# Performance work log

Measured on AMD Instinct MI355X. Metric: run time of the kernel, lower is better.

Reference implementation:

```python
import jax, jax.numpy as jnp
import numpy as np
import math

B, T, D, DI, DFF, H = 4, 1024, 1024, 256, 4096, 16
S, N, E = 16, 256, 1024          # stat_num, token_num, exemplar_len
STAT_K, TOKEN_K = 8, 16
NEG = -1e6


def setup_inputs() -> dict:
    key = jax.random.key(0)
    ks = jax.random.split(key, 32)
    r = lambda i, shape: jax.random.normal(ks[i], shape, jnp.float32)
    w = lambda i, shape: r(i, shape) * 0.02
    return dict(
        x=r(0, (B, T, D)),
        stat_enc=r(1, (B * S, N, D)),
        exemplar_enc=r(2, (B, E, D)),
        stat_feature=r(3, (B, S, D)),
        intent_embed=r(4, (B, 1, DI)),
        Wq1=w(5, (D, D)), Wk1=w(6, (D, D)), Wv1=w(7, (D, D)), Wo1=w(8, (D, D)),
        Wq_stat=w(9, (D + DI, D)), Wq_token=w(10, (D + DI, D)),
        Wk_stat=w(11, (D, D)), Wk_token=w(12, (D, D)),
        Wv_sel=w(13, (D, D)), Wo_sel=w(14, (D, D)),
        Wq2=w(15, (D + DI, D)), Wk2=w(16, (D, D)), Wv2=w(17, (D, D)), Wo2=w(18, (D, D)),
        Wg=w(19, (2 * D, 1)),
        W1=w(20, (D, DFF)), b1=jnp.zeros((DFF,), jnp.float32),
        W2=w(21, (DFF, D)), b2=jnp.zeros((D,), jnp.float32),
        g1=jnp.ones((D,), jnp.float32), be1=jnp.zeros((D,), jnp.float32),
        g2=jnp.ones((D,), jnp.float32), be2=jnp.zeros((D,), jnp.float32),
        g3=jnp.ones((D,), jnp.float32), be3=jnp.zeros((D,), jnp.float32),
        stat_valid_len=jax.random.randint(ks[22], (B,), 1, S + 1),
        example_valid_len=jax.random.randint(ks[23], (B,), 1, E + 1),
    )


def _ln(x, g, b):
    m = x.mean(-1, keepdims=True)
    v = ((x - m) ** 2).mean(-1, keepdims=True)
    return (x - m) / jnp.sqrt(v + 1e-5) * g + b


def _mha(q, k, v, valid, Wq, Wk, Wv, Wo):
    Bq, Tq, _ = q.shape
    Sk = k.shape[1]
    sp = lambda z: z.reshape(Bq, z.shape[1], H, -1).transpose(0, 2, 1, 3)  # B,H,L,dh
    qh, kh, vh = sp(q @ Wq), sp(k @ Wk), sp(v @ Wv)
    dh = qh.shape[-1]
    sc = jnp.einsum('bhtd,bhsd->bhts', qh, kh) / math.sqrt(dh)
    vl = valid[:, None, None, None] if valid.ndim == 1 else valid[:, None, :, None]
    sc = jnp.where(jnp.arange(Sk)[None, None, None, :] < vl, sc, NEG)
    w = jax.nn.softmax(sc, axis=-1)
    out = jnp.einsum('bhts,bhsd->bhtd', w, vh).transpose(0, 2, 1, 3).reshape(Bq, Tq, -1)
    return out @ Wo


def _scatter_topk(scores, k):
    # keep top-k per row, everything else -> NEG (matches torch topk+scatter)
    shp = scores.shape
    flat = scores.reshape(-1, shp[-1])
    vals, idx = jax.lax.top_k(flat, k)
    out = jnp.full_like(flat, NEG).at[jnp.arange(flat.shape[0])[:, None], idx].set(vals)
    return out.reshape(shp)


def reference(x, stat_enc, exemplar_enc, stat_feature, intent_embed,
              Wq1, Wk1, Wv1, Wo1,
              Wq_stat, Wq_token, Wk_stat, Wk_token, Wv_sel, Wo_sel,
              Wq2, Wk2, Wv2, Wo2, Wg,
              W1, b1, W2, b2,
              g1, be1, g2, be2, g3, be3,
              stat_valid_len, example_valid_len):
    # masked self-attention (training mode -> causal valid lens)
    dec_valid = jnp.broadcast_to(jnp.arange(1, T + 1)[None, :], (B, T))
    x2 = _mha(x, x, x, dec_valid, Wq1, Wk1, Wv1, Wo1)
    y = _ln(x + x2, g1, be1)
    yi = jnp.concatenate([y, jnp.broadcast_to(intent_embed, (B, T, DI))], axis=-1)

    # selective hierarchical top-k attention
    qs = yi @ Wq_stat                      # [B,T,D]
    qt = yi @ Wq_token                     # [B,T,D]
    ks = stat_feature @ Wk_stat            # [B,S,D]
    kt = (stat_enc @ Wk_token).reshape(B, S, N, D)
    vv = (stat_enc @ Wv_sel).reshape(B, S, N, D)
    scale = math.sqrt(D)
    ssc = jnp.einsum('btd,bsd->bts', qs, ks) / scale
    ssc = jnp.where(jnp.arange(S)[None, None, :] < stat_valid_len[:, None, None], ssc, NEG)
    sw = jax.nn.softmax(_scatter_topk(ssc, min(S - 1, STAT_K)), axis=-1)   # [B,T,S]
    tsc = jnp.einsum('btd,bsnd->btsn', qt, kt) / scale                      # [B,T,S,N]
    tw = jax.nn.softmax(_scatter_topk(tsc, min(N - 1, TOKEN_K)), axis=-1)
    comb = sw[..., None] * tw                                               # [B,T,S,N]
    y2s = jnp.einsum('btsn,bsnd->btd', comb, vv) @ Wo_sel

    # exemplar cross-attention
    y2e = _mha(yi, exemplar_enc, exemplar_enc, example_valid_len, Wq2, Wk2, Wv2, Wo2)

    gate = jax.nn.sigmoid(jnp.concatenate([y2s, y2e], axis=-1) @ Wg)
    y2 = gate * y2s + (1.0 - gate) * y2e
    z = _ln(y + 2.0 * y2, g2, be2)
    ffn = jax.nn.relu(z @ W1 + b1) @ W2 + b2
    return _ln(z + ffn, g3, be3)
```

## Files before the change

### kernel.cpp

```cpp
#include <hip/hip_runtime.h>

typedef unsigned short u16;
typedef short s16x8 __attribute__((ext_vector_type(8)));
typedef u16 u16x4 __attribute__((ext_vector_type(4)));
typedef float f32x4 __attribute__((ext_vector_type(4)));

#define T_N   1024
#define NEGV  -1e6f
#define MB    (1L << 20)

__device__ __forceinline__ u16 f2bf(float f) {
    unsigned u = __float_as_uint(f);
    u += 0x7fffu + ((u >> 16) & 1u);
    return (u16)(u >> 16);
}
__device__ __forceinline__ float bf2f(u16 h) {
    return __uint_as_float(((unsigned)h) << 16);
}
__device__ __forceinline__ f32x4 mfma16(s16x8 a, s16x8 b, f32x4 c) {
    return __builtin_amdgcn_mfma_f32_16x16x32_bf16(a, b, c, 0, 0, 0);
}
__device__ __forceinline__ void gll16(const u16* g, u16* l) {
    __builtin_amdgcn_global_load_lds((const __attribute__((address_space(1))) void*)g,
                                     (__attribute__((address_space(3))) void*)l, 16, 0, 0);
}

struct P6 { const float* s[6]; u16* d[6]; };

__global__ __launch_bounds__(256) void transpose_cast_batch(P6 pp, int K, int N) {
    const float* __restrict__ src = pp.s[blockIdx.z];
    u16* __restrict__ dst = pp.d[blockIdx.z];
    __shared__ float tile[32][33];
    int nb = blockIdx.x * 32, kb = blockIdx.y * 32;
    int tx = threadIdx.x & 31, ty = threadIdx.x >> 5;
    #pragma unroll
    for (int i = 0; i < 4; i++)
        tile[ty + 8*i][tx] = src[(long)(kb + ty + 8*i) * N + nb + tx];
    __syncthreads();
    #pragma unroll
    for (int i = 0; i < 4; i++)
        dst[(long)(nb + ty + 8*i) * K + kb + tx] = f2bf(tile[tx][ty + 8*i]);
}

__global__ __launch_bounds__(256) void cast_bf16_kernel(const float* __restrict__ src,
                                                        u16* __restrict__ dst, long n) {
    long i = ((long)blockIdx.x * 256 + threadIdx.x) * 4;
    if (i >= n) return;
    float4 v = *(const float4*)(src + i);
    u16x4 o = { f2bf(v.x), f2bf(v.y), f2bf(v.z), f2bf(v.w) };
    *(u16x4*)(dst + i) = o;
}

template<typename OutT, bool RELU, bool HAS_BIAS>
__global__ __launch_bounds__(256) void gemm_bt(
    const u16* __restrict__ A, const u16* __restrict__ Bt, OutT* __restrict__ C,
    const float* __restrict__ bias, int M, int N, int K,
    int lda, int ldb, int ldc,
    int batchDivA, long sA, long sB, long sC)
{
    A  += (long)(blockIdx.z / batchDivA) * sA;
    Bt += (long)blockIdx.z * sB;
    C  += (long)blockIdx.z * sC;
    __shared__ __align__(16) u16 As[4096];
    __shared__ __align__(16) u16 Bs[4096];
    const int tid = threadIdx.x;
    const int wave = tid >> 6, lane = tid & 63;
    const int quad = lane >> 4, l16 = lane & 15;
    const int wr = (wave >> 1) * 64, wc = (wave & 1) * 64;
    const long row0 = (long)blockIdx.y * 128, col0 = (long)blockIdx.x * 128;

    f32x4 acc[4][4] = {};

    const int l4r = lane >> 2;
    const int l4c = (lane & 3) * 8;
    const int ra = wave * 32 + l4r;
    const u16* Ap0 = A + (row0 + ra) * (long)lda + l4c;
    const u16* Ap1 = Ap0 + 16L * lda;
    const u16* Bp0 = Bt + (col0 + ra) * (long)ldb + l4c;
    const u16* Bp1 = Bp0 + 16L * ldb;
    u16* AsW0 = &As[(wave * 32) * 32];
    u16* AsW1 = &As[(wave * 32 + 16) * 32];
    u16* BsW0 = &Bs[(wave * 32) * 32];
    u16* BsW1 = &Bs[(wave * 32 + 16) * 32];
    const bool aok0 = (row0 + wave * 32) < M;
    const bool aok1 = (row0 + wave * 32 + 16) < M;

    for (int k0 = 0; k0 < K; k0 += 32) {
        __syncthreads();
        if (aok0) gll16(Ap0 + k0, AsW0);
        if (aok1) gll16(Ap1 + k0, AsW1);
        gll16(Bp0 + k0, BsW0);
        gll16(Bp1 + k0, BsW1);
        __syncthreads();
        s16x8 af[4], bfr[4];
        #pragma unroll
        for (int i = 0; i < 4; i++)
            af[i]  = *(const s16x8*)&As[(wr + i*16 + l16) * 32 + quad*8];
        #pragma unroll
        for (int j = 0; j < 4; j++)
            bfr[j] = *(const s16x8*)&Bs[(wc + j*16 + l16) * 32 + quad*8];
        #pragma unroll
        for (int i = 0; i < 4; i++)
            #pragma unroll
            for (int j = 0; j < 4; j++)
                acc[i][j] = mfma16(af[i], bfr[j], acc[i][j]);
    }

    #pragma unroll
    for (int i = 0; i < 4; i++) {
        long row = row0 + wr + i*16 + quad*4;
        #pragma unroll
        for (int j = 0; j < 4; j++) {
            long col = col0 + wc + j*16 + l16;
            float bv = 0.f;
            if constexpr (HAS_BIAS) bv = bias[col];
            #pragma unroll
            for (int r = 0; r < 4; r++) {
                if (row + r < M) {
                    float v = acc[i][j][r] + bv;
                    if constexpr (RELU) v = fmaxf(v, 0.f);
                    if constexpr (sizeof(OutT) == 2) C[(row + r) * (long)ldc + col] = f2bf(v);
                    else                             C[(row + r) * (long)ldc + col] = v;
                }
            }
        }
    }
}

template<bool CAUSAL>
__global__ __launch_bounds__(256) void flash_attn_kernel(
    const u16* __restrict__ Q, const u16* __restrict__ Kg, const u16* __restrict__ Vg,
    const int* __restrict__ valid_len, u16* __restrict__ O,
    int qld, int kld, int vld)
{
    const int h = blockIdx.y, b = blockIdx.z;
    const int qt0 = blockIdx.x * 64;
    const int tid = threadIdx.x;
    const int wave = tid >> 6, lane = tid & 63;
    const int quad = lane >> 4, l16 = lane & 15;

    __shared__ __align__(16) u16 Qs[64][72];
    __shared__ __align__(16) u16 Ks[64][72];
    __shared__ __align__(16) u16 Vt[64][72];
    __shared__ __align__(16) u16 Ps[4][16][72];

    const int sr = tid >> 2, scc = (tid & 3) * 16;
    {
        const u16* qp = Q + ((long)b * T_N + qt0 + sr) * qld + h * 64 + scc;
        *(s16x8*)&Qs[sr][scc]     = *(const s16x8*)qp;
        *(s16x8*)&Qs[sr][scc + 8] = *(const s16x8*)(qp + 8);
    }
    float m_i[4] = {-1e30f, -1e30f, -1e30f, -1e30f};
    float l_i[4] = {0.f, 0.f, 0.f, 0.f};
    f32x4 o_acc[4] = {};

    int vl = 0, kend;
    if (CAUSAL) kend = qt0 + 64;
    else { vl = valid_len[b]; kend = (vl + 63) & ~63; }

    for (int kv0 = 0; kv0 < kend; kv0 += 64) {
        __syncthreads();
        {
            const u16* kp = Kg + ((long)b * T_N + kv0 + sr) * kld + h * 64 + scc;
            *(s16x8*)&Ks[sr][scc]     = *(const s16x8*)kp;
            *(s16x8*)&Ks[sr][scc + 8] = *(const s16x8*)(kp + 8);
            const u16* vp = Vg + ((long)b * T_N + kv0 + sr) * vld + h * 64 + scc;
            s16x8 v0 = *(const s16x8*)vp;
            s16x8 v1 = *(const s16x8*)(vp + 8);
            #pragma unroll
            for (int j = 0; j < 8; j++) {
                Vt[scc + j][sr]     = (u16)v0[j];
                Vt[scc + 8 + j][sr] = (u16)v1[j];
            }
        }
        __syncthreads();
        f32x4 sc[4] = {};
        #pragma unroll
        for (int kk = 0; kk < 64; kk += 32) {
            s16x8 aq = *(const s16x8*)&Qs[wave*16 + l16][kk + quad*8];
            #pragma unroll
            for (int j = 0; j < 4; j++) {
                s16x8 bk = *(const s16x8*)&Ks[j*16 + l16][kk + quad*8];
                sc[j] = mfma16(aq, bk, sc[j]);
            }
        }
        const int qrow = qt0 + wave*16 + quad*4;
        #pragma unroll
        for (int j = 0; j < 4; j++) {
            int kcol = kv0 + j*16 + l16;
            #pragma unroll
            for (int r = 0; r < 4; r++) {
                float s = sc[j][r] * 0.125f;
                bool ok = CAUSAL ? (kcol <= qrow + r) : (kcol < vl);
                sc[j][r] = ok ? s : -1e30f;
            }
        }
        float alpha[4];
        #pragma unroll
        for (int r = 0; r < 4; r++) {
            float mx = fmaxf(fmaxf(sc[0][r], sc[1][r]), fmaxf(sc[2][r], sc[3][r]));
            #pragma unroll
            for (int d = 1; d < 16; d <<= 1) mx = fmaxf(mx, __shfl_xor(mx, d, 64));
            float mn = fmaxf(m_i[r], mx);
            alpha[r] = __expf(m_i[r] - mn);
            m_i[r] = mn;
        }
        float rsum[4] = {0.f, 0.f, 0.f, 0.f};
        #pragma unroll
        for (int j = 0; j < 4; j++)
            #pragma unroll
            for (int r = 0; r < 4; r++) {
                float pv = __expf(sc[j][r] - m_i[r]);
                sc[j][r] = pv;
                rsum[r] += pv;
            }
        #pragma unroll
        for (int r = 0; r < 4; r++) {
            #pragma unroll
            for (int d = 1; d < 16; d <<= 1) rsum[r] += __shfl_xor(rsum[r], d, 64);
            l_i[r] = l_i[r] * alpha[r] + rsum[r];
        }
        #pragma unroll
        for (int j = 0; j < 4; j++)
            #pragma unroll
            for (int r = 0; r < 4; r++)
                Ps[wave][quad*4 + r][j*16 + l16] = f2bf(sc[j][r]);
        #pragma unroll
        for (int j2 = 0; j2 < 4; j2++)
            #pragma unroll
            for (int r = 0; r < 4; r++)
                o_acc[j2][r] *= alpha[r];
        __syncthreads();
        #pragma unroll
        for (int kk = 0; kk < 64; kk += 32) {
            s16x8 ap = *(const s16x8*)&Ps[wave][l16][kk + quad*8];
            #pragma unroll
            for (int j2 = 0; j2 < 4; j2++) {
                s16x8 bv = *(const s16x8*)&Vt[j2*16 + l16][kk + quad*8];
                o_acc[j2] = mfma16(ap, bv, o_acc[j2]);
            }
        }
    }
    #pragma unroll
    for (int j2 = 0; j2 < 4; j2++) {
        #pragma unroll
        for (int r = 0; r < 4; r++) {
            float v = o_acc[j2][r] / l_i[r];
            long row = (long)b * T_N + qt0 + wave*16 + quad*4 + r;
            O[row * 1024 + h*64 + j2*16 + l16] = f2bf(v);
        }
    }
}

__global__ __launch_bounds__(256) void ssc_kernel(
    const u16* __restrict__ qs, const u16* __restrict__ ks,
    const int* __restrict__ svl, float* __restrict__ ssc, int qld)
{
    const int t = blockIdx.x, b = blockIdx.y;
    const int wave = threadIdx.x >> 6, lane = threadIdx.x & 63;
    const u16* qrow = qs + ((long)b * T_N + t) * qld + lane * 16;
    const int vl = svl[b];
    for (int s = wave; s < 16; s += 4) {
        const u16* krow = ks + ((long)b * 16 + s) * 1024 + lane * 16;
        float acc = 0.f;
        #pragma unroll
        for (int seg = 0; seg < 2; seg++) {
            s16x8 qv = *(const s16x8*)(qrow + seg*8);
            s16x8 kv = *(const s16x8*)(krow + seg*8);
            #pragma unroll
            for (int j = 0; j < 8; j++) acc += bf2f((u16)qv[j]) * bf2f((u16)kv[j]);
        }
        #pragma unroll
        for (int d = 1; d < 64; d <<= 1) acc += __shfl_xor(acc, d, 64);
        if (lane == 0)
            ssc[((long)b * T_N + t) * 16 + s] = (s < vl) ? acc * (1.f/32.f) : NEGV;
    }
}

__global__ __launch_bounds__(256) void select_combine_kernel(
    const float* __restrict__ ssc, const float* __restrict__ tsc,
    const u16* __restrict__ vv, u16* __restrict__ out, int t0, int vld)
{
    const int tl = blockIdx.x, b = blockIdx.y;
    const int tg = t0 + tl;
    const int tid = threadIdx.x;
    const int wave = tid >> 6, lane = tid & 63;
    __shared__ float coeff[128];
    __shared__ long  rowoff[128];
    __shared__ int   sel_s[8];
    __shared__ float sel_w[8];

    if (wave == 0) {
        float cur = (lane < 16) ? ssc[((long)b * T_N + tg) * 16 + lane] : -3e38f;
        float mx0 = 0.f, ssum = 0.f, myv = -3e38f;
        int myi = 0;
        #pragma unroll
        for (int it = 0; it < 8; it++) {
            float mv = cur; int mi = lane;
            #pragma unroll
            for (int d = 1; d < 64; d <<= 1) {
                float ov = __shfl_xor(mv, d, 64);
                int   oi = __shfl_xor(mi, d, 64);
                if (ov > mv || (ov == mv && oi < mi)) { mv = ov; mi = oi; }
            }
            if (it == 0) mx0 = mv;
            ssum += __expf(mv - mx0);
            if (lane == it) { myv = mv; myi = mi; }
            if (lane == mi) cur = -3e38f;
        }
        if (lane < 8) { sel_s[lane] = myi; sel_w[lane] = __expf(myv - mx0) / ssum; }
    }
    __syncthreads();

    for (int slot = wave; slot < 8; slot += 4) {
        int s = sel_s[slot];
        float sw = sel_w[slot];
        const float* trow = tsc + (((long)b * 16 + s) * 512 + tl) * 256;
        float4 lv4 = *(const float4*)(trow + lane * 4);
        float loc[4] = { lv4.x, lv4.y, lv4.z, lv4.w };
        float mx0 = 0.f, tsum = 0.f, myv = -3e38f;
        int myi = 0;
        for (int it = 0; it < 16; it++) {
            float mv = -3e38f; int mi = 0;
            #pragma unroll
            for (int u = 0; u < 4; u++)
                if (loc[u] > mv) { mv = loc[u]; mi = lane*4 + u; }
            #pragma unroll
            for (int d = 1; d < 64; d <<= 1) {
                float ov = __shfl_xor(mv, d, 64);
                int   oi = __shfl_xor(mi, d, 64);
                if (ov > mv || (ov == mv && oi < mi)) { mv = ov; mi = oi; }
            }
            if (it == 0) mx0 = mv * (1.f/32.f);
            tsum += __expf(mv * (1.f/32.f) - mx0);
            if (lane == it) { myv = mv; myi = mi; }
            if ((mi >> 2) == lane) {
                int u = mi & 3;
                if (u == 0) loc[0] = -3e38f;
                else if (u == 1) loc[1] = -3e38f;
                else if (u == 2) loc[2] = -3e38f;
                else loc[3] = -3e38f;
            }
        }
        if (lane < 16) {
            coeff[slot * 16 + lane]  = sw * __expf(myv * (1.f/32.f) - mx0) / tsum;
            rowoff[slot * 16 + lane] = (long)((b * 16 + s) * 256 + myi) * vld;
        }
    }
    __syncthreads();

    const int d0 = tid * 4;
    float a0 = 0.f, a1 = 0.f, a2 = 0.f, a3 = 0.f;
    for (int r = 0; r < 128; r++) {
        float c = coeff[r];
        const u16* vp = vv + rowoff[r] + d0;
        u16x4 v4 = *(const u16x4*)vp;
        a0 += c * bf2f(v4[0]);
        a1 += c * bf2f(v4[1]);
        a2 += c * bf2f(v4[2]);
        a3 += c * bf2f(v4[3]);
    }
    u16x4 o4 = { f2bf(a0), f2bf(a1), f2bf(a2), f2bf(a3) };
    *(u16x4*)(out + ((long)b * T_N + tg) * 1024 + d0) = o4;
}

__device__ __forceinline__ float block_sum(float v, float* red) {
    #pragma unroll
    for (int d = 1; d < 64; d <<= 1) v += __shfl_xor(v, d, 64);
    __syncthreads();
    if ((threadIdx.x & 63) == 0) red[threadIdx.x >> 6] = v;
    __syncthreads();
    return red[0] + red[1] + red[2] + red[3];
}

__global__ __launch_bounds__(256) void ln1_kernel(
    const float* __restrict__ x, const float* __restrict__ x2,
    const float* __restrict__ intent, const float* __restrict__ g, const float* __restrict__ be,
    u16* __restrict__ yi)
{
    __shared__ float red[4];
    const long row = blockIdx.x;
    const int tid = threadIdx.x;
    const long base = row * 1024 + tid * 4;
    float4 xv = *(const float4*)(x + base);
    float4 dv = *(const float4*)(x2 + base);
    float h0 = xv.x + dv.x, h1 = xv.y + dv.y, h2 = xv.z + dv.z, h3 = xv.w + dv.w;
    float s1 = block_sum(h0 + h1 + h2 + h3, red);
    float s2 = block_sum(h0*h0 + h1*h1 + h2*h2 + h3*h3, red);
    float mean = s1 * (1.f/1024.f);
    float var = s2 * (1.f/1024.f) - mean * mean;
    float inv = rsqrtf(var + 1e-5f);
    const int c = tid * 4;
    float4 gv = *(const float4*)(g + c);
    float4 bv = *(const float4*)(be + c);
    float o0 = (h0 - mean) * inv * gv.x + bv.x;
    float o1 = (h1 - mean) * inv * gv.y + bv.y;
    float o2 = (h2 - mean) * inv * gv.z + bv.z;
    float o3 = (h3 - mean) * inv * gv.w + bv.w;
    u16x4 ob = { f2bf(o0), f2bf(o1), f2bf(o2), f2bf(o3) };
    *(u16x4*)(yi + row * 1280 + c) = ob;
    const int b = (int)(row >> 10);
    yi[row * 1280 + 1024 + tid] = f2bf(intent[b * 256 + tid]);
}

__global__ __launch_bounds__(256) void gate_ln2_kernel(
    const u16* __restrict__ yi, const float* __restrict__ y2s, const float* __restrict__ y2e,
    const float* __restrict__ Wg, const float* __restrict__ g, const float* __restrict__ be,
    float* __restrict__ z, u16* __restrict__ zbf)
{
    __shared__ float red[4];
    const long row = blockIdx.x;
    const int tid = threadIdx.x;
    const long base = row * 1024 + tid * 4;
    const int c = tid * 4;
    float4 sv = *(const float4*)(y2s + base);
    float4 ev = *(const float4*)(y2e + base);
    float4 w1 = *(const float4*)(Wg + c);
    float4 w2 = *(const float4*)(Wg + 1024 + c);
    float dot = sv.x*w1.x + sv.y*w1.y + sv.z*w1.z + sv.w*w1.w
              + ev.x*w2.x + ev.y*w2.y + ev.z*w2.z + ev.w*w2.w;
    float tot = block_sum(dot, red);
    float gate = 1.f / (1.f + __expf(-tot));
    u16x4 yv4 = *(const u16x4*)(yi + row * 1280 + c);
    float h0 = bf2f(yv4[0]) + 2.f * (gate * sv.x + (1.f - gate) * ev.x);
    float h1 = bf2f(yv4[1]) + 2.f * (gate * sv.y + (1.f - gate) * ev.y);
    float h2 = bf2f(yv4[2]) + 2.f * (gate * sv.z + (1.f - gate) * ev.z);
    float h3 = bf2f(yv4[3]) + 2.f * (gate * sv.w + (1.f - gate) * ev.w);
    float s1 = block_sum(h0 + h1 + h2 + h3, red);
    float s2 = block_sum(h0*h0 + h1*h1 + h2*h2 + h3*h3, red);
    float mean = s1 * (1.f/1024.f);
    float var = s2 * (1.f/1024.f) - mean * mean;
    float inv = rsqrtf(var + 1e-5f);
    float4 gv = *(const float4*)(g + c);
    float4 bv = *(const float4*)(be + c);
    float o0 = (h0 - mean) * inv * gv.x + bv.x;
    float o1 = (h1 - mean) * inv * gv.y + bv.y;
    float o2 = (h2 - mean) * inv * gv.z + bv.z;
    float o3 = (h3 - mean) * inv * gv.w + bv.w;
    *(float4*)(z + base) = make_float4(o0, o1, o2, o3);
    u16x4 ob = { f2bf(o0), f2bf(o1), f2bf(o2), f2bf(o3) };
    *(u16x4*)(zbf + row * 1024 + c) = ob;
}

__global__ __launch_bounds__(256) void ln3_kernel(
    const float* __restrict__ z, const float* __restrict__ p0, const float* __restrict__ p1,
    const float* __restrict__ b2,
    const float* __restrict__ g, const float* __restrict__ be, float* __restrict__ out)
{
    __shared__ float red[4];
    const long row = blockIdx.x;
    const int tid = threadIdx.x;
    const long base = row * 1024 + tid * 4;
    const int c = tid * 4;
    float4 zv = *(const float4*)(z + base);
    float4 f0 = *(const float4*)(p0 + base);
    float4 f1 = *(const float4*)(p1 + base);
    float4 bb = *(const float4*)(b2 + c);
    float h0 = zv.x + f0.x + f1.x + bb.x;
    float h1 = zv.y + f0.y + f1.y + bb.y;
    float h2 = zv.z + f0.z + f1.z + bb.z;
    float h3 = zv.w + f0.w + f1.w + bb.w;
    float s1 = block_sum(h0 + h1 + h2 + h3, red);
    float s2 = block_sum(h0*h0 + h1*h1 + h2*h2 + h3*h3, red);
    float mean = s1 * (1.f/1024.f);
    float var = s2 * (1.f/1024.f) - mean * mean;
    float inv = rsqrtf(var + 1e-5f);
    float4 gv = *(const float4*)(g + c);
    float4 bv = *(const float4*)(be + c);
    float o0 = (h0 - mean) * inv * gv.x + bv.x;
    float o1 = (h1 - mean) * inv * gv.y + bv.y;
    float o2 = (h2 - mean) * inv * gv.z + bv.z;
    float o3 = (h3 - mean) * inv * gv.w + bv.w;
    *(float4*)(out + base) = make_float4(o0, o1, o2, o3);
}

extern "C" void kernel_launch(void* const* d_in, const int* in_sizes, int n_in,
                              void* d_out, int out_size, void* d_ws, size_t ws_size,
                              hipStream_t stream)
{
    (void)in_sizes; (void)n_in; (void)out_size; (void)ws_size;
    const float* x      = (const float*)d_in[0];
    const float* stat_e = (const float*)d_in[1];
    const float* exem   = (const float*)d_in[2];
    const float* sfeat  = (const float*)d_in[3];
    const float* intent = (const float*)d_in[4];
    const float* Wg  = (const float*)d_in[19];
    const float* b1  = (const float*)d_in[21];
    const float* b2  = (const float*)d_in[23];
    const float* g1  = (const float*)d_in[24]; const float* be1 = (const float*)d_in[25];
    const float* g2  = (const float*)d_in[26]; const float* be2 = (const float*)d_in[27];
    const float* g3  = (const float*)d_in[28]; const float* be3 = (const float*)d_in[29];
    const int* svl = (const int*)d_in[30];
    const int* evl = (const int*)d_in[31];
    float* outp = (float*)d_out;

    char* base = (char*)d_ws;
    u16*  bufA  = (u16*)(base + 0*MB);
    u16*  qkv1  = (u16*)(base + 8*MB);
    float* x2a  = (float*)(base + 8*MB);
    u16*  kv2   = (u16*)(base + 8*MB);
    u16*  w1t   = (u16*)(base + 8*MB);
    u16*  w2t   = (u16*)(base + 16*MB);
    u16*  yibf  = (u16*)(base + 32*MB);
    u16*  buf3  = (u16*)(base + 42*MB);
    u16*  zbf   = (u16*)(base + 42*MB);
    u16*  sebf  = (u16*)(base + 66*MB);
    float* tsch = (float*)(base + 66*MB);
    u16*  hid   = (u16*)(base + 66*MB);
    u16*  ktvv  = (u16*)(base + 98*MB);
    float* y2sf = (float*)(base + 98*MB);
    float* p0f  = (float*)(base + 98*MB);
    u16*  exbf  = (u16*)(base + 114*MB);
    float* y2ef = (float*)(base + 122*MB);
    float* zf   = (float*)(base + 138*MB);
    u16*  sfbf  = (u16*)(base + 162*MB);
    u16*  ksbf  = (u16*)(base + 162*MB + 256*1024);
    float* sscf = (float*)(base + 162*MB + 512*1024);
    char* wpool = base + 163*MB;

    dim3 blk(256);
    auto cast = [&](const float* s, u16* d, long n) {
        cast_bf16_kernel<<<dim3((unsigned)((n/4 + 255) / 256)), blk, 0, stream>>>(s, d, n);
    };
    auto g_n = [&](const u16* A, const u16* Bt, u16* C, int M, int N, int K,
                   int lda, int ldb, int ldc) {
        gemm_bt<u16,false,false><<<dim3(N/128, (M+127)/128, 1), blk, 0, stream>>>(
            A, Bt, C, nullptr, M, N, K, lda, ldb, ldc, 1, 0, 0, 0);
    };
    auto g_f = [&](const u16* A, const u16* Bt, float* C, int M, int N, int K,
                   int lda, int ldb, int ldc) {
        gemm_bt<float,false,false><<<dim3(N/128, (M+127)/128, 1), blk, 0, stream>>>(
            A, Bt, C, nullptr, M, N, K, lda, ldb, ldc, 1, 0, 0, 0);
    };

    u16* wqkv1t = (u16*)wpool;
    u16* wo1t   = (u16*)(wpool) + 3L*1024*1024;
    {
        P6 pp{};
        pp.s[0]=(const float*)d_in[5]; pp.d[0]=wqkv1t;
        pp.s[1]=(const float*)d_in[6]; pp.d[1]=wqkv1t + 1L*1024*1024;
        pp.s[2]=(const float*)d_in[7]; pp.d[2]=wqkv1t + 2L*1024*1024;
        pp.s[3]=(const float*)d_in[8]; pp.d[3]=wo1t;
        transpose_cast_batch<<<dim3(32, 32, 4), blk, 0, stream>>>(pp, 1024, 1024);
    }
    cast(x, bufA, 4096L*1024);
    g_n(bufA, wqkv1t, qkv1, 4096, 3072, 1024, 1024, 1024, 3072);
    flash_attn_kernel<true><<<dim3(16, 16, 4), blk, 0, stream>>>(
        qkv1, qkv1 + 1024, qkv1 + 2048, nullptr, bufA, 3072, 3072, 3072);
    g_f(bufA, wo1t, x2a, 4096, 1024, 1024, 1024, 1024, 1024);
    ln1_kernel<<<dim3(4096), blk, 0, stream>>>(x, x2a, intent, g1, be1, yibf);

    u16* wq3t = (u16*)wpool;
    {
        P6 pp{};
        pp.s[0]=(const float*)d_in[9];  pp.d[0]=wq3t;
        pp.s[1]=(const float*)d_in[10]; pp.d[1]=wq3t + 1L*1024*1280;
        pp.s[2]=(const float*)d_in[15]; pp.d[2]=wq3t + 2L*1024*1280;
        transpose_cast_batch<<<dim3(32, 40, 3), blk, 0, stream>>>(pp, 1280, 1024);
    }
    g_n(yibf, wq3t, buf3, 4096, 3072, 1280, 1280, 1280, 3072);
    u16* wkst = (u16*)wpool;
    u16* wkv  = (u16*)(wpool) + 1L*1024*1024;
    {
        P6 pp{};
        pp.s[0]=(const float*)d_in[11]; pp.d[0]=wkst;
        pp.s[1]=(const float*)d_in[12]; pp.d[1]=wkv;
        pp.s[2]=(const float*)d_in[13]; pp.d[2]=wkv + 1L*1024*1024;
        transpose_cast_batch<<<dim3(32, 32, 3), blk, 0, stream>>>(pp, 1024, 1024);
    }
    cast(sfeat, sfbf, 64L*1024);
    cast(stat_e, sebf, 16384L*1024);
    g_n(sfbf, wkst, ksbf, 64, 1024, 1024, 1024, 1024, 1024);
    g_n(sebf, wkv, ktvv, 16384, 2048, 1024, 1024, 1024, 2048);
    ssc_kernel<<<dim3(1024, 4), blk, 0, stream>>>(buf3, ksbf, svl, sscf, 3072);
    for (int hh = 0; hh < 2; hh++) {
        long t0 = hh * 512;
        gemm_bt<float,false,false><<<dim3(2, 4, 64), blk, 0, stream>>>(
            buf3 + 1024 + t0*3072, ktvv, tsch, nullptr, 512, 256, 1024,
            3072, 2048, 256, 16, (long)T_N*3072, 256L*2048, 512L*256);
        select_combine_kernel<<<dim3(512, 4), blk, 0, stream>>>(
            sscf, tsch, ktvv + 1024, bufA, (int)t0, 2048);
    }
    u16* wost = (u16*)wpool;
    u16* wkv2 = (u16*)(wpool) + 1L*1024*1024;
    u16* wo2t = (u16*)(wpool) + 3L*1024*1024;
    {
        P6 pp{};
        pp.s[0]=(const float*)d_in[14]; pp.d[0]=wost;
        pp.s[1]=(const float*)d_in[16]; pp.d[1]=wkv2;
        pp.s[2]=(const float*)d_in[17]; pp.d[2]=wkv2 + 1L*1024*1024;
        pp.s[3]=(const float*)d_in[18]; pp.d[3]=wo2t;
        transpose_cast_batch<<<dim3(32, 32, 4), blk, 0, stream>>>(pp, 1024, 1024);
    }
    g_f(bufA, wost, y2sf, 4096, 1024, 1024, 1024, 1024, 1024);

    cast(exem, exbf, 4096L*1024);
    g_n(exbf, wkv2, kv2, 4096, 2048, 1024, 1024, 1024, 2048);
    flash_attn_kernel<false><<<dim3(16, 16, 4), blk, 0, stream>>>(
        buf3 + 2048, kv2, kv2 + 1024, evl, bufA, 3072, 2048, 2048);
    g_f(bufA, wo2t, y2ef, 4096, 1024, 1024, 1024, 1024, 1024);

    gate_ln2_kernel<<<dim3(4096), blk, 0, stream>>>(yibf, y2sf, y2ef, Wg, g2, be2, zf, zbf);

    {
        P6 pp{}; pp.s[0] = (const float*)d_in[20]; pp.d[0] = w1t;
        transpose_cast_batch<<<dim3(128, 32, 1), blk, 0, stream>>>(pp, 1024, 4096);
    }
    {
        P6 pp{}; pp.s[0] = (const float*)d_in[22]; pp.d[0] = w2t;
        transpose_cast_batch<<<dim3(32, 128, 1), blk, 0, stream>>>(pp, 4096, 1024);
    }
    gemm_bt<u16,true,true><<<dim3(32, 32, 1), blk, 0, stream>>>(
        zbf, w1t, hid, b1, 4096, 4096, 1024, 1024, 1024, 4096, 1, 0, 0, 0);
    gemm_bt<float,false,false><<<dim3(8, 32, 2), blk, 0, stream>>>(
        hid, w2t, p0f, nullptr, 4096, 1024, 2048, 4096, 4096, 1024,
        1, 2048, 2048, 4096L*1024);

    ln3_kernel<<<dim3(4096), blk, 0, stream>>>(zf, p0f, p0f + 4096L*1024, b2, g3, be3, outp);
}
```

Baseline: 1.032 ms.

## Split-K output projections, batch weight casts, and swizzle GEMM block order

The three 1024x1024 output-projection GEMMs (attention, selection, exemplar) each become two half-K launches writing partial fp32 sums, and the following LayerNorm/gate kernels add the partials. This raises the block count from 256 to 512 per projection for better CU occupancy. Weight transpose-casts and input casts are merged into fewer batched launches with per-slice shapes, and the GEMM gets a grid swizzle of the block index to improve L2 reuse. The workspace layout is reshuffled to hold the extra partial buffers, which costs extra memory traffic for the partial outputs.

```diff
diff --git a/kernel.cpp b/kernel.cpp
--- a/kernel.cpp
+++ b/kernel.cpp
@@ -25,13 +25,16 @@
                                      (__attribute__((address_space(3))) void*)l, 16, 0, 0);
 }
 
-struct P6 { const float* s[6]; u16* d[6]; };
-
-__global__ __launch_bounds__(256) void transpose_cast_batch(P6 pp, int K, int N) {
-    const float* __restrict__ src = pp.s[blockIdx.z];
-    u16* __restrict__ dst = pp.d[blockIdx.z];
+struct T8 { const float* s[8]; u16* d[8]; int K[8]; int N[8]; };
+
+__global__ __launch_bounds__(256) void transpose_cast_b(T8 pp) {
+    const int z = blockIdx.z;
+    const int K = pp.K[z], N = pp.N[z];
+    int nb = blockIdx.x * 32, kb = blockIdx.y * 32;
+    if (nb >= N || kb >= K) return;
+    const float* __restrict__ src = pp.s[z];
+    u16* __restrict__ dst = pp.d[z];
     __shared__ float tile[32][33];
-    int nb = blockIdx.x * 32, kb = blockIdx.y * 32;
     int tx = threadIdx.x & 31, ty = threadIdx.x >> 5;
     #pragma unroll
     for (int i = 0; i < 4; i++)
@@ -42,6 +45,18 @@
         dst[(long)(nb + ty + 8*i) * K + kb + tx] = f2bf(tile[tx][ty + 8*i]);
 }
 
+struct C4 { const float* s[4]; u16* d[4]; long n[4]; };
+
+__global__ __launch_bounds__(256) void cast_batch_kernel(C4 c) {
+    long i = ((long)blockIdx.x * 256 + threadIdx.x) * 4;
+    if (i >= c.n[blockIdx.z]) return;
+    const float* __restrict__ src = c.s[blockIdx.z];
+    u16* __restrict__ dst = c.d[blockIdx.z];
+    float4 v = *(const float4*)(src + i);
+    u16x4 o = { f2bf(v.x), f2bf(v.y), f2bf(v.z), f2bf(v.w) };
+    *(u16x4*)(dst + i) = o;
+}
+
 __global__ __launch_bounds__(256) void cast_bf16_kernel(const float* __restrict__ src,
                                                         u16* __restrict__ dst, long n) {
     long i = ((long)blockIdx.x * 256 + threadIdx.x) * 4;
@@ -61,13 +76,25 @@
     A  += (long)(blockIdx.z / batchDivA) * sA;
     Bt += (long)blockIdx.z * sB;
     C  += (long)blockIdx.z * sC;
+
+    int bx = blockIdx.x, by = blockIdx.y;
+    {
+        const int nb = gridDim.x * gridDim.y;
+        if ((nb & 7) == 0) {
+            int flat = by * gridDim.x + bx;
+            int nf = (flat & 7) * (nb >> 3) + (flat >> 3);
+            bx = nf % gridDim.x;
+            by = nf / gridDim.x;
+        }
+    }
+
     __shared__ __align__(16) u16 As[4096];
     __shared__ __align__(16) u16 Bs[4096];
     const int tid = threadIdx.x;
     const int wave = tid >> 6, lane = tid & 63;
     const int quad = lane >> 4, l16 = lane & 15;
     const int wr = (wave >> 1) * 64, wc = (wave & 1) * 64;
-    const long row0 = (long)blockIdx.y * 128, col0 = (long)blockIdx.x * 128;
+    const long row0 = (long)by * 128, col0 = (long)bx * 128;
 
     f32x4 acc[4][4] = {};
 
@@ -374,7 +401,7 @@
 }
 
 __global__ __launch_bounds__(256) void ln1_kernel(
-    const float* __restrict__ x, const float* __restrict__ x2,
+    const float* __restrict__ x, const float* __restrict__ p0, const float* __restrict__ p1,
     const float* __restrict__ intent, const float* __restrict__ g, const float* __restrict__ be,
     u16* __restrict__ yi)
 {
@@ -383,8 +410,10 @@
     const int tid = threadIdx.x;
     const long base = row * 1024 + tid * 4;
     float4 xv = *(const float4*)(x + base);
-    float4 dv = *(const float4*)(x2 + base);
-    float h0 = xv.x + dv.x, h1 = xv.y + dv.y, h2 = xv.z + dv.z, h3 = xv.w + dv.w;
+    float4 d0 = *(const float4*)(p0 + base);
+    float4 d1 = *(const float4*)(p1 + base);
+    float h0 = xv.x + d0.x + d1.x, h1 = xv.y + d0.y + d1.y;
+    float h2 = xv.z + d0.z + d1.z, h3 = xv.w + d0.w + d1.w;
     float s1 = block_sum(h0 + h1 + h2 + h3, red);
     float s2 = block_sum(h0*h0 + h1*h1 + h2*h2 + h3*h3, red);
     float mean = s1 * (1.f/1024.f);
@@ -404,7 +433,9 @@
 }
 
 __global__ __launch_bounds__(256) void gate_ln2_kernel(
-    const u16* __restrict__ yi, const float* __restrict__ y2s, const float* __restrict__ y2e,
+    const u16* __restrict__ yi,
+    const float* __restrict__ s0p, const float* __restrict__ s1p,
+    const float* __restrict__ e0p, const float* __restrict__ e1p,
     const float* __restrict__ Wg, const float* __restrict__ g, const float* __restrict__ be,
     float* __restrict__ z, u16* __restrict__ zbf)
 {
@@ -413,8 +444,12 @@
     const int tid = threadIdx.x;
     const long base = row * 1024 + tid * 4;
     const int c = tid * 4;
-    float4 sv = *(const float4*)(y2s + base);
-    float4 ev = *(const float4*)(y2e + base);
+    float4 sa = *(const float4*)(s0p + base);
+    float4 sb = *(const float4*)(s1p + base);
+    float4 ea = *(const float4*)(e0p + base);
+    float4 eb = *(const float4*)(e1p + base);
+    float4 sv = make_float4(sa.x + sb.x, sa.y + sb.y, sa.z + sb.z, sa.w + sb.w);
+    float4 ev = make_float4(ea.x + eb.x, ea.y + eb.y, ea.z + eb.z, ea.w + eb.w);
     float4 w1 = *(const float4*)(Wg + c);
     float4 w2 = *(const float4*)(Wg + 1024 + c);
     float dot = sv.x*w1.x + sv.y*w1.y + sv.z*w1.z + sv.w*w1.w
@@ -497,79 +532,87 @@
     char* base = (char*)d_ws;
     u16*  bufA  = (u16*)(base + 0*MB);
     u16*  qkv1  = (u16*)(base + 8*MB);
-    float* x2a  = (float*)(base + 8*MB);
+    float* p0x  = (float*)(base + 8*MB);
+    u16*  wq3t  = (u16*)(base + 8*MB);
+    u16*  wkst  = (u16*)(base + 8*MB + 7864320L);
+    u16*  wkv   = (u16*)(base + 8*MB + 9961472L);
+    u16*  wost  = (u16*)(base + 8*MB + 14155776L);
     u16*  kv2   = (u16*)(base + 8*MB);
-    u16*  w1t   = (u16*)(base + 8*MB);
-    u16*  w2t   = (u16*)(base + 16*MB);
+    float* zf   = (float*)(base + 8*MB);
     u16*  yibf  = (u16*)(base + 32*MB);
+    float* p1x  = (float*)(base + 42*MB);
     u16*  buf3  = (u16*)(base + 42*MB);
     u16*  zbf   = (u16*)(base + 42*MB);
+    u16*  w1t   = (u16*)(base + 50*MB);
+    u16*  w2t   = (u16*)(base + 58*MB);
     u16*  sebf  = (u16*)(base + 66*MB);
     float* tsch = (float*)(base + 66*MB);
     u16*  hid   = (u16*)(base + 66*MB);
     u16*  ktvv  = (u16*)(base + 98*MB);
-    float* y2sf = (float*)(base + 98*MB);
-    float* p0f  = (float*)(base + 98*MB);
-    u16*  exbf  = (u16*)(base + 114*MB);
-    float* y2ef = (float*)(base + 122*MB);
-    float* zf   = (float*)(base + 138*MB);
+    float* ys0  = (float*)(base + 98*MB);
+    float* ys1  = (float*)(base + 114*MB);
+    float* ye0  = (float*)(base + 130*MB);
+    float* ye1  = (float*)(base + 146*MB);
+    float* f0p  = (float*)(base + 98*MB);
     u16*  sfbf  = (u16*)(base + 162*MB);
     u16*  ksbf  = (u16*)(base + 162*MB + 256*1024);
     float* sscf = (float*)(base + 162*MB + 512*1024);
     char* wpool = base + 163*MB;
 
     dim3 blk(256);
-    auto cast = [&](const float* s, u16* d, long n) {
-        cast_bf16_kernel<<<dim3((unsigned)((n/4 + 255) / 256)), blk, 0, stream>>>(s, d, n);
-    };
     auto g_n = [&](const u16* A, const u16* Bt, u16* C, int M, int N, int K,
                    int lda, int ldb, int ldc) {
         gemm_bt<u16,false,false><<<dim3(N/128, (M+127)/128, 1), blk, 0, stream>>>(
             A, Bt, C, nullptr, M, N, K, lda, ldb, ldc, 1, 0, 0, 0);
     };
-    auto g_f = [&](const u16* A, const u16* Bt, float* C, int M, int N, int K,
-                   int lda, int ldb, int ldc) {
-        gemm_bt<float,false,false><<<dim3(N/128, (M+127)/128, 1), blk, 0, stream>>>(
-            A, Bt, C, nullptr, M, N, K, lda, ldb, ldc, 1, 0, 0, 0);
+    auto g_sk = [&](const u16* A, const u16* Bt, float* P, int lda) {
+        gemm_bt<float,false,false><<<dim3(8, 32, 2), blk, 0, stream>>>(
+            A, Bt, P, nullptr, 4096, 1024, 512, lda, 1024, 1024,
+            1, 512, 512, 4096L*1024);
     };
+
+    {
+        C4 cc{};
+        cc.s[0] = stat_e; cc.d[0] = sebf; cc.n[0] = 16384L*1024;
+        cc.s[1] = x;      cc.d[1] = bufA; cc.n[1] = 4096L*1024;
+        cc.s[2] = sfeat;  cc.d[2] = sfbf; cc.n[2] = 64L*1024;
+        cast_batch_kernel<<<dim3(16384, 1, 3), blk, 0, stream>>>(cc);
+    }
 
     u16* wqkv1t = (u16*)wpool;
     u16* wo1t   = (u16*)(wpool) + 3L*1024*1024;
     {
-        P6 pp{};
+        T8 pp{};
         pp.s[0]=(const float*)d_in[5]; pp.d[0]=wqkv1t;
         pp.s[1]=(const float*)d_in[6]; pp.d[1]=wqkv1t + 1L*1024*1024;
         pp.s[2]=(const float*)d_in[7]; pp.d[2]=wqkv1t + 2L*1024*1024;
         pp.s[3]=(const float*)d_in[8]; pp.d[3]=wo1t;
-        transpose_cast_batch<<<dim3(32, 32, 4), blk, 0, stream>>>(pp, 1024, 1024);
-    }
-    cast(x, bufA, 4096L*1024);
+        for (int i = 0; i < 4; i++) { pp.K[i] = 1024; pp.N[i] = 1024; }
+        transpose_cast_b<<<dim3(32, 32, 4), blk, 0, stream>>>(pp);
+    }
     g_n(bufA, wqkv1t, qkv1, 4096, 3072, 1024, 1024, 1024, 3072);
     flash_attn_kernel<true><<<dim3(16, 16, 4), blk, 0, stream>>>(
         qkv1, qkv1 + 1024, qkv1 + 2048, nullptr, bufA, 3072, 3072, 3072);
-    g_f(bufA, wo1t, x2a, 4096, 1024, 1024, 1024, 1024, 1024);
-    ln1_kernel<<<dim3(4096), blk, 0, stream>>>(x, x2a, intent, g1, be1, yibf);
-
-    u16* wq3t = (u16*)wpool;
-    {
-        P6 pp{};
-        pp.s[0]=(const float*)d_in[9];  pp.d[0]=wq3t;
-        pp.s[1]=(const float*)d_in[10]; pp.d[1]=wq3t + 1L*1024*1280;
-        pp.s[2]=(const float*)d_in[15]; pp.d[2]=wq3t + 2L*1024*1280;
-        transpose_cast_batch<<<dim3(32, 40, 3), blk, 0, stream>>>(pp, 1280, 1024);
+    {
+        gemm_bt<float,false,false><<<dim3(8, 32, 1), blk, 0, stream>>>(
+            bufA, wo1t, p0x, nullptr, 4096, 1024, 512, 1024, 1024, 1024, 1, 0, 0, 0);
+        gemm_bt<float,false,false><<<dim3(8, 32, 1), blk, 0, stream>>>(
+            bufA + 512, wo1t + 512, p1x, nullptr, 4096, 1024, 512, 1024, 1024, 1024, 1, 0, 0, 0);
+    }
+    ln1_kernel<<<dim3(4096), blk, 0, stream>>>(x, p0x, p1x, intent, g1, be1, yibf);
+
+    {
+        T8 pp{};
+        pp.s[0]=(const float*)d_in[9];  pp.d[0]=wq3t;                    pp.K[0]=1280; pp.N[0]=1024;
+        pp.s[1]=(const float*)d_in[10]; pp.d[1]=wq3t + 1L*1024*1280;     pp.K[1]=1280; pp.N[1]=1024;
+        pp.s[2]=(const float*)d_in[15]; pp.d[2]=wq3t + 2L*1024*1280;     pp.K[2]=1280; pp.N[2]=1024;
+        pp.s[3]=(const float*)d_in[11]; pp.d[3]=wkst;                    pp.K[3]=1024; pp.N[3]=1024;
+        pp.s[4]=(const float*)d_in[12]; pp.d[4]=wkv;                     pp.K[4]=1024; pp.N[4]=1024;
+        pp.s[5]=(const float*)d_in[13]; pp.d[5]=wkv + 1L*1024*1024;      pp.K[5]=1024; pp.N[5]=1024;
+        pp.s[6]=(const float*)d_in[14]; pp.d[6]=wost;                    pp.K[6]=1024; pp.N[6]=1024;
+        transpose_cast_b<<<dim3(32, 40, 7), blk, 0, stream>>>(pp);
     }
     g_n(yibf, wq3t, buf3, 4096, 3072, 1280, 1280, 1280, 3072);
-    u16* wkst = (u16*)wpool;
-    u16* wkv  = (u16*)(wpool) + 1L*1024*1024;
-    {
-        P6 pp{};
-        pp.s[0]=(const float*)d_in[11]; pp.d[0]=wkst;
-        pp.s[1]=(const float*)d_in[12]; pp.d[1]=wkv;
-        pp.s[2]=(const float*)d_in[13]; pp.d[2]=wkv + 1L*1024*1024;
-        transpose_cast_batch<<<dim3(32, 32, 3), blk, 0, stream>>>(pp, 1024, 1024);
-    }
-    cast(sfeat, sfbf, 64L*1024);
-    cast(stat_e, sebf, 16384L*1024);
     g_n(sfbf, wkst, ksbf, 64, 1024, 1024, 1024, 1024, 1024);
     g_n(sebf, wkv, ktvv, 16384, 2048, 1024, 1024, 1024, 2048);
     ssc_kernel<<<dim3(1024, 4), blk, 0, stream>>>(buf3, ksbf, svl, sscf, 3072);
@@ -581,40 +624,52 @@
         select_combine_kernel<<<dim3(512, 4), blk, 0, stream>>>(
             sscf, tsch, ktvv + 1024, bufA, (int)t0, 2048);
     }
-    u16* wost = (u16*)wpool;
-    u16* wkv2 = (u16*)(wpool) + 1L*1024*1024;
-    u16* wo2t = (u16*)(wpool) + 3L*1024*1024;
-    {
-        P6 pp{};
-        pp.s[0]=(const float*)d_in[14]; pp.d[0]=wost;
-        pp.s[1]=(const float*)d_in[16]; pp.d[1]=wkv2;
-        pp.s[2]=(const float*)d_in[17]; pp.d[2]=wkv2 + 1L*1024*1024;
-        pp.s[3]=(const float*)d_in[18]; pp.d[3]=wo2t;
-        transpose_cast_batch<<<dim3(32, 32, 4), blk, 0, stream>>>(pp, 1024, 1024);
-    }
-    g_f(bufA, wost, y2sf, 4096, 1024, 1024, 1024, 1024, 1024);
-
-    cast(exem, exbf, 4096L*1024);
-    g_n(exbf, wkv2, kv2, 4096, 2048, 1024, 1024, 1024, 2048);
+    {
+        gemm_bt<float,false,false><<<dim3(8, 32, 1), blk, 0, stream>>>(
+            bufA, wost, ys0, nullptr, 4096, 1024, 512, 1024, 1024, 1024, 1, 0, 0, 0);
+        gemm_bt<float,false,false><<<dim3(8, 32, 1), blk, 0, stream>>>(
+            bufA + 512, wost + 512, ys1, nullptr, 4096, 1024, 512, 1024, 1024, 1024, 1, 0, 0, 0);
+    }
+
+    u16* wkv2 = (u16*)wpool;
+    u16* wo2t = (u16*)(wpool) + 2L*1024*1024;
+    {
+        T8 pp{};
+        pp.s[0]=(const float*)d_in[16]; pp.d[0]=wkv2;
+        pp.s[1]=(const float*)d_in[17]; pp.d[1]=wkv2 + 1L*1024*1024;
+        pp.s[2]=(const float*)d_in[18]; pp.d[2]=wo2t;
+        for (int i = 0; i < 3; i++) { pp.K[i] = 1024; pp.N[i] = 1024; }
+        transpose_cast_b<<<dim3(32, 32, 3), blk, 0, stream>>>(pp);
+    }
+    cast_bf16_kernel<<<dim3(4096), blk, 0, stream>>>(exem, bufA, 4096L*1024);
+    g_n(bufA, wkv2, kv2, 4096, 2048, 1024, 1024, 1024, 2048);
     flash_attn_kernel<false><<<dim3(16, 16, 4), blk, 0, stream>>>(
         buf3 + 2048, kv2, kv2 + 1024, evl, bufA, 3072, 2048, 2048);
-    g_f(bufA, wo2t, y2ef, 4096, 1024, 1024, 1024, 1024, 1024);
-
-    gate_ln2_kernel<<<dim3(4096), blk, 0, stream>>>(yibf, y2sf, y2ef, Wg, g2, be2, zf, zbf);
-
-    {
-        P6 pp{}; pp.s[0] = (const float*)d_in[20]; pp.d[0] = w1t;
-        transpose_cast_batch<<<dim3(128, 32, 1), blk, 0, stream>>>(pp, 1024, 4096);
-    }
-    {
-        P6 pp{}; pp.s[0] = (const float*)d_in[22]; pp.d[0] = w2t;
-        transpose_cast_batch<<<dim3(32, 128, 1), blk, 0, stream>>>(pp, 4096, 1024);
+    {
+        gemm_bt<float,false,false><<<dim3(8, 32, 1), blk, 0, stream>>>(
+            bufA, wo2t, ye0, nullptr, 4096, 1024, 512, 1024, 1024, 1024, 1, 0, 0, 0);
+        gemm_bt<float,false,false><<<dim3(8, 32, 1), blk, 0, stream>>>(
+            bufA + 512, wo2t + 512, ye1, nullptr, 4096, 1024, 512, 1024, 1024, 1024, 1, 0, 0, 0);
+    }
+
+    gate_ln2_kernel<<<dim3(4096), blk, 0, stream>>>(
+        yibf, ys0, ys1, ye0, ye1, Wg, g2, be2, zf, zbf);
+
+    {
+        T8 pp{}; pp.s[0] = (const float*)d_in[20]; pp.d[0] = w1t;
+        pp.K[0] = 1024; pp.N[0] = 4096;
+        transpose_cast_b<<<dim3(128, 32, 1), blk, 0, stream>>>(pp);
+    }
+    {
+        T8 pp{}; pp.s[0] = (const float*)d_in[22]; pp.d[0] = w2t;
+        pp.K[0] = 4096; pp.N[0] = 1024;
+        transpose_cast_b<<<dim3(32, 128, 1), blk, 0, stream>>>(pp);
     }
     gemm_bt<u16,true,true><<<dim3(32, 32, 1), blk, 0, stream>>>(
         zbf, w1t, hid, b1, 4096, 4096, 1024, 1024, 1024, 4096, 1, 0, 0, 0);
     gemm_bt<float,false,false><<<dim3(8, 32, 2), blk, 0, stream>>>(
-        hid, w2t, p0f, nullptr, 4096, 1024, 2048, 4096, 4096, 1024,
+        hid, w2t, f0p, nullptr, 4096, 1024, 2048, 4096, 4096, 1024,
         1, 2048, 2048, 4096L*1024);
 
-    ln3_kernel<<<dim3(4096), blk, 0, stream>>>(zf, p0f, p0f + 4096L*1024, b2, g3, be3, outp);
-}
+    ln3_kernel<<<dim3(4096), blk, 0, stream>>>(zf, f0p, f0p + 4096L*1024, b2, g3, be3, outp);
+}
```

New measurement: 1.036 ms. Within noise of the previous version (+0.4%).
